# Performance work log

Measured on AMD Instinct MI355X. Metric: run time of the kernel, lower is better.

The kernel has to match this reference:

```python
import jax, jax.numpy as jnp
import numpy as np

B, S, D = 2, 2048, 2048
H = 16
Q_LORA, KV_LORA = 1536, 512
ROPE_DIM, NOPE_DIM, V_DIM = 64, 64, 128
Q_HEAD_DIM = NOPE_DIM + ROPE_DIM  # 128
ROPE_THETA, ROPE_RATIO = 10000.0, 1.0


def setup_inputs() -> dict:
    key = jax.random.key(0)
    ks = jax.random.split(key, 6)
    std = 0.02
    return {
        "hidden_states": jax.random.normal(ks[0], (B, S, D), jnp.float32),
        "Wqa": jax.random.normal(ks[1], (D, Q_LORA), jnp.float32) * std,
        "Wqb": jax.random.normal(ks[2], (Q_LORA, H * Q_HEAD_DIM), jnp.float32) * std,
        "Wkva": jax.random.normal(ks[3], (D, KV_LORA + ROPE_DIM), jnp.float32) * std,
        "Wkvb": jax.random.normal(ks[4], (KV_LORA, H * (NOPE_DIM + V_DIM)), jnp.float32) * std,
        "Wo": jax.random.normal(ks[5], (H * V_DIM, D), jnp.float32) * std,
    }


def _rope_tables(seq_len):
    half = ROPE_DIM // 2
    inv_freq = ROPE_RATIO / (ROPE_THETA ** (jnp.arange(half, dtype=jnp.float32) * 2.0 / ROPE_DIM))
    freqs = jnp.arange(seq_len, dtype=jnp.float32)[:, None] * inv_freq[None, :]  # [S, half]
    return jnp.cos(freqs), jnp.sin(freqs)


def _apply_rope(x, cos, sin):
    # interleaved even/odd rotation, matches torch stack+flatten
    x_even = x[..., 0::2]
    x_odd = x[..., 1::2]
    r_even = x_even * cos - x_odd * sin
    r_odd = x_odd * cos + x_even * sin
    return jnp.stack([r_even, r_odd], axis=-1).reshape(x.shape)


def reference(hidden_states, Wqa, Wqb, Wkva, Wkvb, Wo):
    b, s, _ = hidden_states.shape
    scale = Q_HEAD_DIM ** -0.5

    # query compression path
    q_latent = hidden_states @ Wqa                             # [B,S,Q_LORA]
    q = (q_latent @ Wqb).reshape(b, s, H, Q_HEAD_DIM)
    q = jnp.transpose(q, (0, 2, 1, 3))                          # [B,H,S,q_head_dim]
    q_nope, q_pe = q[..., :NOPE_DIM], q[..., NOPE_DIM:]

    # kv compression
    kv_comp = hidden_states @ Wkva                              # [B,S,KV_LORA+ROPE]
    c_kv, k_pe = kv_comp[..., :KV_LORA], kv_comp[..., KV_LORA:]

    cos, sin = _rope_tables(s)                                  # [S, ROPE_DIM//2]
    q_pe = _apply_rope(q_pe, cos, sin)                          # [B,H,S,ROPE]
    k_pe = _apply_rope(k_pe, cos, sin)                          # [B,S,ROPE]

    # kv decompression
    kv = (c_kv @ Wkvb).reshape(b, s, H, NOPE_DIM + V_DIM)
    kv = jnp.transpose(kv, (0, 2, 1, 3))                        # [B,H,S,nope+v]
    k_nope, v = kv[..., :NOPE_DIM], kv[..., NOPE_DIM:]

    k_pe_b = jnp.broadcast_to(k_pe[:, None], (b, H, s, ROPE_DIM))
    q_full = jnp.concatenate([q_nope, q_pe], axis=-1)           # [B,H,S,128]
    k_full = jnp.concatenate([k_nope, k_pe_b], axis=-1)         # [B,H,S,128]

    scores = jnp.einsum('bhqd,bhkd->bhqk', q_full, k_full) * scale
    causal = jnp.tril(jnp.ones((s, s), dtype=bool))
    scores = jnp.where(causal[None, None], scores, jnp.finfo(scores.dtype).min)
    probs = jax.nn.softmax(scores, axis=-1)
    attn = jnp.einsum('bhqk,bhkd->bhqd', probs, v)              # [B,H,S,V_DIM]

    out = jnp.transpose(attn, (0, 2, 1, 3)).reshape(b, s, H * V_DIM)
    return out @ Wo                                             # [B,S,D]
```

## Files before the change

### kernel.cpp

```cpp
#include <hip/hip_runtime.h>
#include <hip/hip_bf16.h>
#include <cstdint>
#include <cstddef>

typedef __bf16 bf16_t;
typedef __attribute__((ext_vector_type(8))) __bf16 bf16x8;
typedef __attribute__((ext_vector_type(4))) float f32x4;

#define S_ 2048
#define H_ 16
#define NTOK 4096

__device__ __forceinline__ f32x4 mfma16x16(bf16x8 a, bf16x8 b, f32x4 c) {
  return __builtin_amdgcn_mfma_f32_16x16x32_bf16(a, b, c, 0, 0, 0);
}
__device__ __forceinline__ bf16x8 load8(const bf16_t* p) {
  return *reinterpret_cast<const bf16x8*>(p);
}
__device__ __forceinline__ void load_lds16(const void* g, void* l) {
  __builtin_amdgcn_global_load_lds(
      (const __attribute__((address_space(1))) uint32_t*)g,
      (__attribute__((address_space(3))) uint32_t*)l, 16, 0, 0);
}


__global__ void cast_bf16_k(const float* __restrict__ in, bf16_t* __restrict__ out, int n) {
  int idx = blockIdx.x * 256 + threadIdx.x;
  int i4 = idx * 4;
  if (i4 >= n) return;
  float4 v = *reinterpret_cast<const float4*>(in + i4);
  out[i4 + 0] = (bf16_t)v.x;
  out[i4 + 1] = (bf16_t)v.y;
  out[i4 + 2] = (bf16_t)v.z;
  out[i4 + 3] = (bf16_t)v.w;
}

__global__ void transpose_cast_k(const float* __restrict__ in, bf16_t* __restrict__ out,
                                 int K, int Nsrc, int Nout) {
  __shared__ float tile[32][33];
  int k0 = blockIdx.y * 32, n0 = blockIdx.x * 32;
  int tx = threadIdx.x & 31, ty = threadIdx.x >> 5;
#pragma unroll
  for (int i = 0; i < 4; ++i) {
    int k = k0 + ty + i * 8, n = n0 + tx;
    tile[ty + i * 8][tx] = (n < Nsrc) ? in[(size_t)k * Nsrc + n] : 0.0f;
  }
  __syncthreads();
#pragma unroll
  for (int i = 0; i < 4; ++i) {
    int n = n0 + ty + i * 8, k = k0 + tx;
    out[(size_t)n * K + k] = (bf16_t)tile[tx][ty + i * 8];
  }
}

__global__ void transpose_v_k(const bf16_t* __restrict__ kv, bf16_t* __restrict__ vT) {
  __shared__ bf16_t tile[32][33];
  int bh = blockIdx.z;
  int b = bh >> 4, h = bh & 15;
  int s0 = blockIdx.x * 32, d0 = blockIdx.y * 32;
  int tx = threadIdx.x & 31, ty = threadIdx.x >> 5;
#pragma unroll
  for (int i = 0; i < 4; ++i) {
    int s = s0 + ty + i * 8;
    tile[ty + i * 8][tx] = kv[(size_t)(b * S_ + s) * 3072 + h * 192 + 64 + d0 + tx];
  }
  __syncthreads();
#pragma unroll
  for (int i = 0; i < 4; ++i) {
    int d = d0 + ty + i * 8;
    vT[((size_t)bh * 128 + d) * 2048 + s0 + tx] = tile[tx][ty + i * 8];
  }
}

__global__ void rope_tables_k(float* __restrict__ cosT, float* __restrict__ sinT) {
  int idx = blockIdx.x * 256 + threadIdx.x;
  if (idx >= S_ * 32) return;
  int s = idx >> 5, i = idx & 31;
  float inv = powf(10000.0f, -(2.0f * (float)i) / 64.0f);
  float fr = (float)s * inv;
  cosT[idx] = cosf(fr);
  sinT[idx] = sinf(fr);
}

__global__ void rope_apply_k(bf16_t* __restrict__ buf, const float* __restrict__ cosT,
                             const float* __restrict__ sinT, int ld, int nh, int hstride, int off) {
  int idx = blockIdx.x * 256 + threadIdx.x;
  int total = NTOK * nh * 32;
  if (idx >= total) return;
  int i = idx & 31;
  int h = (idx >> 5) % nh;
  int t = idx / (32 * nh);
  int s = t & (S_ - 1);
  float c = cosT[s * 32 + i], sn = sinT[s * 32 + i];
  bf16_t* p = buf + (size_t)t * ld + off + h * hstride + 2 * i;
  float xe = (float)p[0], xo = (float)p[1];
  p[0] = (bf16_t)(xe * c - xo * sn);
  p[1] = (bf16_t)(xo * c + xe * sn);
}


template <int OUT_F32>
__global__ __launch_bounds__(256) void gemm_bf16(const bf16_t* __restrict__ A, int lda,
                                                 const bf16_t* __restrict__ Bt,
                                                 void* __restrict__ Cv, int M, int N, int K,
                                                 float scale) {
  __shared__ alignas(16) bf16_t Al[128 * 32];
  __shared__ alignas(16) bf16_t Bl[128 * 32];
  const int tid = threadIdx.x;
  const int wid = tid >> 6, lane = tid & 63;
  const int m0 = blockIdx.y * 128, n0 = blockIdx.x * 128;
  const int wm = (wid >> 1) * 64, wn = (wid & 1) * 64;

  f32x4 acc[4][4] = {};

  const int srow = wid * 32 + (lane >> 2);
  const int scol = (lane & 3) * 8;
  const bf16_t* ag0 = A + (size_t)(m0 + srow) * lda + scol;
  const bf16_t* ag1 = A + (size_t)(m0 + srow + 16) * lda + scol;
  const bf16_t* bg0 = Bt + (size_t)(n0 + srow) * K + scol;
  const bf16_t* bg1 = Bt + (size_t)(n0 + srow + 16) * K + scol;
  bf16_t* al0 = &Al[wid * 1024];
  bf16_t* al1 = &Al[wid * 1024 + 512];
  bf16_t* bl0 = &Bl[wid * 1024];
  bf16_t* bl1 = &Bl[wid * 1024 + 512];

  const int lr = lane & 15, lk = (lane >> 4) * 8;

  for (int k0 = 0; k0 < K; k0 += 32) {
    load_lds16(ag0 + k0, al0);
    load_lds16(ag1 + k0, al1);
    load_lds16(bg0 + k0, bl0);
    load_lds16(bg1 + k0, bl1);
    __syncthreads();
    bf16x8 af[4], bfr[4];
#pragma unroll
    for (int i = 0; i < 4; ++i) {
      af[i] = load8(&Al[(wm + i * 16 + lr) * 32 + lk]);
      bfr[i] = load8(&Bl[(wn + i * 16 + lr) * 32 + lk]);
    }
#pragma unroll
    for (int i = 0; i < 4; ++i)
#pragma unroll
      for (int j = 0; j < 4; ++j) acc[i][j] = mfma16x16(af[i], bfr[j], acc[i][j]);
    __syncthreads();
  }

  const int lg = lane >> 4;
  if (OUT_F32) {
    float* C = (float*)Cv;
#pragma unroll
    for (int i = 0; i < 4; ++i)
#pragma unroll
      for (int j = 0; j < 4; ++j)
#pragma unroll
        for (int r = 0; r < 4; ++r) {
          int row = m0 + wm + i * 16 + lg * 4 + r;
          int col = n0 + wn + j * 16 + lr;
          C[(size_t)row * N + col] = acc[i][j][r] * scale;
        }
  } else {
    bf16_t* C = (bf16_t*)Cv;
#pragma unroll
    for (int i = 0; i < 4; ++i)
#pragma unroll
      for (int j = 0; j < 4; ++j)
#pragma unroll
        for (int r = 0; r < 4; ++r) {
          int row = m0 + wm + i * 16 + lg * 4 + r;
          int col = n0 + wn + j * 16 + lr;
          C[(size_t)row * N + col] = (bf16_t)(acc[i][j][r] * scale);
        }
  }
}

__global__ __launch_bounds__(256) void attn_fused(const bf16_t* __restrict__ q,
                                                  const bf16_t* __restrict__ kv,
                                                  const bf16_t* __restrict__ lat,
                                                  const bf16_t* __restrict__ vT,
                                                  bf16_t* __restrict__ out) {
  __shared__ alignas(16) bf16_t Kn[64 * 64];
  __shared__ alignas(16) bf16_t Kp[64 * 64];
  __shared__ alignas(16) bf16_t Vt[128 * 64];
  __shared__ alignas(16) bf16_t Pl[4][16 * 64];
  const int tid = threadIdx.x, wid = tid >> 6, lane = tid & 63;
  const int bid = blockIdx.x;
  const int g = bid >> 8;
  const int x = (bid >> 5) & 7;
  const int bh = bid & 31;
  const int qt = (g & 1) ? (24 - g * 8 + x) : (31 - g * 8 - x);
  const int b = bh >> 4, h = bh & 15;
  const int tokb = b * S_;
  const int lr = lane & 15, lg = lane >> 4;
  const int srow8 = lane >> 3, c8 = lane & 7;
  const int swz8 = c8 ^ srow8;
  bf16_t* Pw = &Pl[wid][0];

  bf16x8 qf[4];
  {
    const int qrow = qt * 64 + wid * 16 + lr;
    const bf16_t* qp = q + (size_t)(tokb + qrow) * 2048 + h * 128 + lg * 8;
#pragma unroll
    for (int ds = 0; ds < 4; ++ds) qf[ds] = load8(qp + ds * 32);
  }

  f32x4 o[8] = {};
  float mrow[4] = {-1e30f, -1e30f, -1e30f, -1e30f};
  float lrow[4] = {0.f, 0.f, 0.f, 0.f};

  for (int t = 0; t <= qt; ++t) {
    const int kb = t * 64;
#pragma unroll
    for (int rr = 0; rr < 2; ++rr) {
      const int r0 = wid * 16 + rr * 8;
      const size_t tk = (size_t)(tokb + kb + r0 + srow8);
      load_lds16(kv + tk * 3072 + h * 192 + (swz8 << 3), &Kn[r0 * 64]);
      load_lds16(lat + tk * 2176 + 2048 + (swz8 << 3), &Kp[r0 * 64]);
    }
#pragma unroll
    for (int rr = 0; rr < 4; ++rr) {
      const int r0 = wid * 32 + rr * 8;
      load_lds16(vT + ((size_t)bh * 128 + r0 + srow8) * 2048 + kb + (swz8 << 3), &Vt[r0 * 64]);
    }
    __syncthreads();

    f32x4 s[4];
    __builtin_amdgcn_s_setprio(1);
#pragma unroll
    for (int kt = 0; kt < 4; ++kt) {
      const int row = kt * 16 + lr;
      const int e = lr & 7;
      bf16x8 kf0 = load8(&Kn[row * 64 + ((lg ^ e) << 3)]);
      bf16x8 kf1 = load8(&Kn[row * 64 + (((lg + 4) ^ e) << 3)]);
      bf16x8 kf2 = load8(&Kp[row * 64 + ((lg ^ e) << 3)]);
      bf16x8 kf3 = load8(&Kp[row * 64 + (((lg + 4) ^ e) << 3)]);
      f32x4 acc = {0.f, 0.f, 0.f, 0.f};
      acc = mfma16x16(qf[0], kf0, acc);
      acc = mfma16x16(qf[1], kf1, acc);
      acc = mfma16x16(qf[2], kf2, acc);
      acc = mfma16x16(qf[3], kf3, acc);
      s[kt] = acc;
    }
    __builtin_amdgcn_s_setprio(0);

    if (t == qt) {
#pragma unroll
      for (int kt = 0; kt < 4; ++kt) {
        const int key = kb + kt * 16 + lr;
#pragma unroll
        for (int r = 0; r < 4; ++r) {
          const int qr = qt * 64 + wid * 16 + lg * 4 + r;
          if (key > qr) s[kt][r] = -1e30f;
        }
      }
    }

    float tm[4];
#pragma unroll
    for (int r = 0; r < 4; ++r) {
      float mx = fmaxf(fmaxf(s[0][r], s[1][r]), fmaxf(s[2][r], s[3][r]));
      mx = fmaxf(mx, __shfl_xor(mx, 1));
      mx = fmaxf(mx, __shfl_xor(mx, 2));
      mx = fmaxf(mx, __shfl_xor(mx, 4));
      mx = fmaxf(mx, __shfl_xor(mx, 8));
      tm[r] = mx;
    }
    float need = fmaxf(fmaxf(tm[0] - mrow[0], tm[1] - mrow[1]),
                       fmaxf(tm[2] - mrow[2], tm[3] - mrow[3]));
    if (!__all(need <= 8.0f)) {
#pragma unroll
      for (int r = 0; r < 4; ++r) {
        float mn = fmaxf(mrow[r], tm[r]);
        float corr = exp2f(mrow[r] - mn);
        mrow[r] = mn;
        lrow[r] *= corr;
#pragma unroll
        for (int n = 0; n < 8; ++n) o[n][r] *= corr;
      }
    }
    float psum[4] = {0.f, 0.f, 0.f, 0.f};
#pragma unroll
    for (int kt = 0; kt < 4; ++kt)
#pragma unroll
      for (int r = 0; r < 4; ++r) {
        float p = exp2f(s[kt][r] - mrow[r]);
        s[kt][r] = p;
        psum[r] += p;
      }
#pragma unroll
    for (int r = 0; r < 4; ++r) {
      float ps = psum[r];
      ps += __shfl_xor(ps, 1);
      ps += __shfl_xor(ps, 2);
      ps += __shfl_xor(ps, 4);
      ps += __shfl_xor(ps, 8);
      lrow[r] += ps;
    }

#pragma unroll
    for (int kt = 0; kt < 4; ++kt)
#pragma unroll
      for (int r = 0; r < 4; ++r) {
        const int qrow = lg * 4 + r;
        const int key = kt * 16 + lr;
        Pw[qrow * 64 + ((((key >> 3) ^ (qrow & 7)) << 3) | (key & 7))] = (bf16_t)s[kt][r];
      }

    __builtin_amdgcn_s_setprio(1);
#pragma unroll
    for (int ks = 0; ks < 2; ++ks) {
      const int e = lr & 7;
      bf16x8 pa = load8(&Pw[lr * 64 + (((ks * 4 + lg) ^ e) << 3)]);
#pragma unroll
      for (int n = 0; n < 8; ++n) {
        bf16x8 vb = load8(&Vt[(n * 16 + lr) * 64 + (((ks * 4 + lg) ^ e) << 3)]);
        o[n] = mfma16x16(pa, vb, o[n]);
      }
    }
    __builtin_amdgcn_s_setprio(0);
    __syncthreads();
  }

  float linv[4];
#pragma unroll
  for (int r = 0; r < 4; ++r) linv[r] = __builtin_amdgcn_rcpf(lrow[r]);
#pragma unroll
  for (int n = 0; n < 8; ++n)
#pragma unroll
    for (int r = 0; r < 4; ++r) {
      const int qr = qt * 64 + wid * 16 + lg * 4 + r;
      out[(size_t)(tokb + qr) * 2048 + h * 128 + n * 16 + lr] = (bf16_t)(o[n][r] * linv[r]);
    }
}


extern "C" void kernel_launch(void* const* d_in, const int* in_sizes, int n_in, void* d_out,
                              int out_size, void* d_ws, size_t ws_size, hipStream_t stream) {
  const float* hs = (const float*)d_in[0];
  const float* Wqa = (const float*)d_in[1];
  const float* Wqb = (const float*)d_in[2];
  const float* Wkva = (const float*)d_in[3];
  const float* Wkvb = (const float*)d_in[4];
  const float* Wo = (const float*)d_in[5];
  float* out = (float*)d_out;

  char* ws = (char*)d_ws;
  size_t off = 0;
  auto alloc = [&](size_t bytes) {
    void* p = ws + off;
    off += (bytes + 255) & ~(size_t)255;
    return p;
  };
  bf16_t* hsb = (bf16_t*)alloc((size_t)NTOK * 2048 * 2);
  bf16_t* W1t = (bf16_t*)alloc((size_t)2176 * 2048 * 2);
  bf16_t* Wqbt = (bf16_t*)alloc((size_t)2048 * 1536 * 2);
  bf16_t* Wkvbt = (bf16_t*)alloc((size_t)3072 * 512 * 2);
  bf16_t* Wot = (bf16_t*)alloc((size_t)2048 * 2048 * 2);
  bf16_t* lat = (bf16_t*)alloc((size_t)NTOK * 2176 * 2);
  bf16_t* qb = (bf16_t*)alloc((size_t)NTOK * 2048 * 2);
  bf16_t* kvb = (bf16_t*)alloc((size_t)NTOK * 3072 * 2);
  bf16_t* attn = (bf16_t*)alloc((size_t)NTOK * 2048 * 2);
  bf16_t* vT = (bf16_t*)alloc((size_t)32 * 128 * 2048 * 2);
  float* cosT = (float*)alloc((size_t)S_ * 32 * 4);
  float* sinT = (float*)alloc((size_t)S_ * 32 * 4);

  cast_bf16_k<<<(NTOK * 2048 / 4 + 255) / 256, 256, 0, stream>>>(hs, hsb, NTOK * 2048);
  transpose_cast_k<<<dim3(1536 / 32, 2048 / 32), 256, 0, stream>>>(Wqa, W1t, 2048, 1536, 1536);
  transpose_cast_k<<<dim3(640 / 32, 2048 / 32), 256, 0, stream>>>(Wkva, W1t + (size_t)1536 * 2048,
                                                                  2048, 576, 640);
  transpose_cast_k<<<dim3(2048 / 32, 1536 / 32), 256, 0, stream>>>(Wqb, Wqbt, 1536, 2048, 2048);
  transpose_cast_k<<<dim3(3072 / 32, 512 / 32), 256, 0, stream>>>(Wkvb, Wkvbt, 512, 3072, 3072);
  transpose_cast_k<<<dim3(2048 / 32, 2048 / 32), 256, 0, stream>>>(Wo, Wot, 2048, 2048, 2048);
  rope_tables_k<<<(S_ * 32 + 255) / 256, 256, 0, stream>>>(cosT, sinT);

  gemm_bf16<0><<<dim3(2176 / 128, NTOK / 128), 256, 0, stream>>>(hsb, 2048, W1t, lat, NTOK, 2176,
                                                                 2048, 1.0f);
  rope_apply_k<<<(NTOK * 32 + 255) / 256, 256, 0, stream>>>(lat, cosT, sinT, 2176, 1, 0, 2048);
  const float scale = 0.08838834764831845f * 1.4426950408889634f;
  gemm_bf16<0><<<dim3(2048 / 128, NTOK / 128), 256, 0, stream>>>(lat, 2176, Wqbt, qb, NTOK, 2048,
                                                                 1536, scale);
  rope_apply_k<<<(NTOK * 16 * 32 + 255) / 256, 256, 0, stream>>>(qb, cosT, sinT, 2048, 16, 128, 64);
  gemm_bf16<0><<<dim3(3072 / 128, NTOK / 128), 256, 0, stream>>>(lat + 1536, 2176, Wkvbt, kvb, NTOK,
                                                                 3072, 512, 1.0f);
  transpose_v_k<<<dim3(64, 4, 32), 256, 0, stream>>>(kvb, vT);
  attn_fused<<<dim3(1024), 256, 0, stream>>>(qb, kvb, lat, vT, attn);
  gemm_bf16<1><<<dim3(2048 / 128, NTOK / 128), 256, 0, stream>>>(attn, 2048, Wot, out, NTOK, 2048,
                                                                 2048, 1.0f);
}
```

Before: 325.9 us.

## Batch weight transposes into one launch and compute softmax row sums via MFMA

New measurement: 309.1 us. -5.1%, faster.

```diff
diff --git a/kernel.cpp b/kernel.cpp
--- a/kernel.cpp
+++ b/kernel.cpp
@@ -35,21 +35,39 @@
   out[i4 + 3] = (bf16_t)v.w;
 }
 
-__global__ void transpose_cast_k(const float* __restrict__ in, bf16_t* __restrict__ out,
-                                 int K, int Nsrc, int Nout) {
+struct TDesc {
+  const float* src;
+  bf16_t* dst;
+  int K, Nsrc, bxc, off;
+};
+struct TDesc5 {
+  TDesc d[5];
+};
+
+__global__ void transpose_cast_multi_k(TDesc5 ds) {
   __shared__ float tile[32][33];
-  int k0 = blockIdx.y * 32, n0 = blockIdx.x * 32;
+  const int bid = blockIdx.x;
+  int i = 0;
+#pragma unroll
+  for (int j = 1; j < 5; ++j)
+    if (bid >= ds.d[j].off) i = j;
+  const float* __restrict__ in = ds.d[i].src;
+  bf16_t* __restrict__ out = ds.d[i].dst;
+  const int K = ds.d[i].K, Nsrc = ds.d[i].Nsrc;
+  const int local = bid - ds.d[i].off;
+  const int n0 = (local % ds.d[i].bxc) * 32;
+  const int k0 = (local / ds.d[i].bxc) * 32;
   int tx = threadIdx.x & 31, ty = threadIdx.x >> 5;
 #pragma unroll
-  for (int i = 0; i < 4; ++i) {
-    int k = k0 + ty + i * 8, n = n0 + tx;
-    tile[ty + i * 8][tx] = (n < Nsrc) ? in[(size_t)k * Nsrc + n] : 0.0f;
+  for (int r = 0; r < 4; ++r) {
+    int k = k0 + ty + r * 8, n = n0 + tx;
+    tile[ty + r * 8][tx] = (n < Nsrc) ? in[(size_t)k * Nsrc + n] : 0.0f;
   }
   __syncthreads();
 #pragma unroll
-  for (int i = 0; i < 4; ++i) {
-    int n = n0 + ty + i * 8, k = k0 + tx;
-    out[(size_t)n * K + k] = (bf16_t)tile[tx][ty + i * 8];
+  for (int r = 0; r < 4; ++r) {
+    int n = n0 + ty + r * 8, k = k0 + tx;
+    out[(size_t)n * K + k] = (bf16_t)tile[tx][ty + r * 8];
   }
 }
 
@@ -195,6 +213,10 @@
   const int swz8 = c8 ^ srow8;
   bf16_t* Pw = &Pl[wid][0];
 
+  bf16x8 ones;
+#pragma unroll
+  for (int j = 0; j < 8; ++j) ones[j] = (bf16_t)1.0f;
+
   bf16x8 qf[4];
   {
     const int qrow = qt * 64 + wid * 16 + lr;
@@ -204,8 +226,8 @@
   }
 
   f32x4 o[8] = {};
+  f32x4 o8 = {};
   float mrow[4] = {-1e30f, -1e30f, -1e30f, -1e30f};
-  float lrow[4] = {0.f, 0.f, 0.f, 0.f};
 
   for (int t = 0; t <= qt; ++t) {
     const int kb = t * 64;
@@ -272,29 +294,15 @@
         float mn = fmaxf(mrow[r], tm[r]);
         float corr = exp2f(mrow[r] - mn);
         mrow[r] = mn;
-        lrow[r] *= corr;
+        o8[r] *= corr;
 #pragma unroll
         for (int n = 0; n < 8; ++n) o[n][r] *= corr;
       }
     }
-    float psum[4] = {0.f, 0.f, 0.f, 0.f};
 #pragma unroll
     for (int kt = 0; kt < 4; ++kt)
 #pragma unroll
-      for (int r = 0; r < 4; ++r) {
-        float p = exp2f(s[kt][r] - mrow[r]);
-        s[kt][r] = p;
-        psum[r] += p;
-      }
-#pragma unroll
-    for (int r = 0; r < 4; ++r) {
-      float ps = psum[r];
-      ps += __shfl_xor(ps, 1);
-      ps += __shfl_xor(ps, 2);
-      ps += __shfl_xor(ps, 4);
-      ps += __shfl_xor(ps, 8);
-      lrow[r] += ps;
-    }
+      for (int r = 0; r < 4; ++r) s[kt][r] = exp2f(s[kt][r] - mrow[r]);
 
 #pragma unroll
     for (int kt = 0; kt < 4; ++kt)
@@ -315,6 +323,7 @@
         bf16x8 vb = load8(&Vt[(n * 16 + lr) * 64 + (((ks * 4 + lg) ^ e) << 3)]);
         o[n] = mfma16x16(pa, vb, o[n]);
       }
+      o8 = mfma16x16(pa, ones, o8);
     }
     __builtin_amdgcn_s_setprio(0);
     __syncthreads();
@@ -322,7 +331,7 @@
 
   float linv[4];
 #pragma unroll
-  for (int r = 0; r < 4; ++r) linv[r] = __builtin_amdgcn_rcpf(lrow[r]);
+  for (int r = 0; r < 4; ++r) linv[r] = __builtin_amdgcn_rcpf(o8[r]);
 #pragma unroll
   for (int n = 0; n < 8; ++n)
 #pragma unroll
@@ -364,12 +373,21 @@
   float* sinT = (float*)alloc((size_t)S_ * 32 * 4);
 
   cast_bf16_k<<<(NTOK * 2048 / 4 + 255) / 256, 256, 0, stream>>>(hs, hsb, NTOK * 2048);
-  transpose_cast_k<<<dim3(1536 / 32, 2048 / 32), 256, 0, stream>>>(Wqa, W1t, 2048, 1536, 1536);
-  transpose_cast_k<<<dim3(640 / 32, 2048 / 32), 256, 0, stream>>>(Wkva, W1t + (size_t)1536 * 2048,
-                                                                  2048, 576, 640);
-  transpose_cast_k<<<dim3(2048 / 32, 1536 / 32), 256, 0, stream>>>(Wqb, Wqbt, 1536, 2048, 2048);
-  transpose_cast_k<<<dim3(3072 / 32, 512 / 32), 256, 0, stream>>>(Wkvb, Wkvbt, 512, 3072, 3072);
-  transpose_cast_k<<<dim3(2048 / 32, 2048 / 32), 256, 0, stream>>>(Wo, Wot, 2048, 2048, 2048);
+  {
+    TDesc5 ds;
+    int o0 = 0;
+    auto add = [&](int i, const float* src, bf16_t* dst, int K, int Nsrc, int Nout) {
+      int bxc = Nout / 32, cnt = bxc * (K / 32);
+      ds.d[i] = TDesc{src, dst, K, Nsrc, bxc, o0};
+      o0 += cnt;
+    };
+    add(0, Wqa, W1t, 2048, 1536, 1536);
+    add(1, Wkva, W1t + (size_t)1536 * 2048, 2048, 576, 640);
+    add(2, Wqb, Wqbt, 1536, 2048, 2048);
+    add(3, Wkvb, Wkvbt, 512, 3072, 3072);
+    add(4, Wo, Wot, 2048, 2048, 2048);
+    transpose_cast_multi_k<<<o0, 256, 0, stream>>>(ds);
+  }
   rope_tables_k<<<(S_ * 32 + 255) / 256, 256, 0, stream>>>(cosT, sinT);
 
   gemm_bf16<0><<<dim3(2176 / 128, NTOK / 128), 256, 0, stream>>>(hsb, 2048, W1t, lat, NTOK, 2176,
```
